# Kernel tuning notes

Measured on AMD Instinct MI355X. Metric: run time of the kernel, lower is better.

## Reference

```python
import jax, jax.numpy as jnp
import numpy as np

B, S, D_IN, UNITS = 4, 4096, 256, 64


def setup_inputs() -> dict:
    key = jax.random.key(0)
    ks = jax.random.split(key, 4)
    scale = 1.0 / np.sqrt(D_IN)
    return {
        "x": jax.random.normal(ks[0], (B, S, D_IN), dtype=jnp.float32),
        "Wq": jax.random.normal(ks[1], (D_IN, UNITS), dtype=jnp.float32) * scale,
        "bq": jnp.zeros((UNITS,), dtype=jnp.float32),
        "Wk": jax.random.normal(ks[2], (D_IN, UNITS), dtype=jnp.float32) * scale,
        "bk": jnp.zeros((UNITS,), dtype=jnp.float32),
        "Wv": jax.random.normal(ks[3], (D_IN, UNITS), dtype=jnp.float32) * scale,
        "bv": jnp.zeros((UNITS,), dtype=jnp.float32),
    }


def reference(x, Wq, bq, Wk, bk, Wv, bv):
    # Q/K/V projections: [B, S, D_IN] @ [D_IN, UNITS] -> [B, S, UNITS]
    q = jnp.einsum("bsd,du->bsu", x, Wq) + bq
    k = jnp.einsum("bsd,du->bsu", x, Wk) + bk
    v = jnp.einsum("bsd,du->bsu", x, Wv) + bv
    # Full [B, S, S] scores (the module materializes these - headroom target)
    sims = jnp.einsum("bsu,btu->bst", q, k) / np.sqrt(UNITS).astype(np.float32)
    attn = jax.nn.softmax(sims, axis=-1)
    out = jnp.einsum("bst,btu->bsu", attn, v)
    return out  # activation is None (linear)
```

## Files before the change

kernel.cpp:

```cpp
#include <hip/hip_runtime.h>
#include <hip/hip_bf16.h>

#define B_ 4
#define S_ 4096
#define D_ 256
#define U_ 64
#define NROWS (B_ * S_)
#define QSCALE 0.1803368801111244f

typedef __attribute__((ext_vector_type(8))) short short8;
typedef __attribute__((ext_vector_type(8))) float float8;
typedef __attribute__((ext_vector_type(4))) float floatx4;

__device__ inline short f2bf(float f) {
    union { __hip_bfloat16 h; short s; } u;
    u.h = __float2bfloat16(f);
    return u.s;
}
__device__ inline unsigned pk2bf(float a, float b) {
    unsigned ua = __float_as_uint(a) + 0x8000u;
    unsigned ub = __float_as_uint(b) + 0x8000u;
    return (ub & 0xFFFF0000u) | (ua >> 16);
}
__device__ inline float fast_exp2(float x) {
#if __has_builtin(__builtin_amdgcn_exp2f)
    return __builtin_amdgcn_exp2f(x);
#else
    return exp2f(x);
#endif
}

__global__ void pack_w_kernel(const float* __restrict__ Wq,
                              const float* __restrict__ Wk,
                              const float* __restrict__ Wv,
                              short* __restrict__ wpack) {
    int tid = blockIdx.x * 256 + threadIdx.x;
    if (tid >= 3 * 16384) return;
    int p = tid >> 14, e = tid & 16383;
    const float* W = (p == 0) ? Wq : (p == 1) ? Wk : Wv;
    float w = W[e];
    int k = e >> 6, n = e & 63;
    int ks = k >> 5, hi = (k >> 3) & 3, j = k & 7;
    int l = hi * 16 + (n & 15), nc = n >> 4;
    wpack[p * 16384 + ((ks * 4 + nc) * 64 + l) * 8 + j] = f2bf(w);
}

__global__ __launch_bounds__(256) void qkv_proj_kernel(
    const float* __restrict__ x, const short* __restrict__ wpack,
    const float* __restrict__ bq, const float* __restrict__ bk,
    const float* __restrict__ bv,
    short* __restrict__ Q, short* __restrict__ Kpack, short* __restrict__ Vpack) {
    __shared__ __align__(16) short k_sh[64][72];
    __shared__ __align__(16) short vT_sh[64][72];
    const int wl    = threadIdx.x >> 6;
    const int lane  = threadIdx.x & 63;
    const int col16 = lane & 15, quad = lane >> 4;
    const int m0b = blockIdx.x * 64, m0 = m0b + wl * 16;

    floatx4 acc[3][4];
#pragma unroll
    for (int p = 0; p < 3; ++p)
#pragma unroll
        for (int nc = 0; nc < 4; ++nc) acc[p][nc] = (floatx4){0.f, 0.f, 0.f, 0.f};

    const float* xrow = x + (size_t)(m0 + col16) * D_ + quad * 8;
#pragma unroll
    for (int ks = 0; ks < 8; ++ks) {
        float8 af = *(const float8*)(xrow + ks * 32);
        short8 a;
#pragma unroll
        for (int j = 0; j < 8; ++j) a[j] = f2bf(af[j]);
#pragma unroll
        for (int p = 0; p < 3; ++p) {
#pragma unroll
            for (int nc = 0; nc < 4; ++nc) {
                short8 bfr = *(const short8*)(wpack +
                    ((size_t)((p * 8 + ks) * 4 + nc) * 64 + lane) * 8);
                acc[p][nc] = __builtin_amdgcn_mfma_f32_16x16x32_bf16(a, bfr, acc[p][nc], 0, 0, 0);
            }
        }
    }

#pragma unroll
    for (int nc = 0; nc < 4; ++nc) {
        float biasq = bq[nc * 16 + col16];
        float biask = bk[nc * 16 + col16];
        float biasv = bv[nc * 16 + col16];
#pragma unroll
        for (int r = 0; r < 4; ++r) {
            int row = m0 + quad * 4 + r;
            Q[(size_t)row * U_ + nc * 16 + col16] = f2bf((acc[0][nc][r] + biasq) * QSCALE);
            k_sh[wl * 16 + quad * 4 + r][nc * 16 + col16] = f2bf(acc[1][nc][r] + biask);
        }
        union { short s[4]; unsigned long long u; } pv;
#pragma unroll
        for (int r = 0; r < 4; ++r) pv.s[r] = f2bf(acc[2][nc][r] + biasv);
        *(unsigned long long*)&vT_sh[nc * 16 + col16][wl * 16 + quad * 4] = pv.u;
    }
    __syncthreads();

#pragma unroll
    for (int c2 = 0; c2 < 2; ++c2) {
        int combo = wl + c2 * 4;
        int ww = combo >> 2, t = (combo >> 1) & 1, h = combo & 1;
        int srow = ww * 32 + (col16 >> 2) * 8 + (col16 & 3) + 4 * t;
        short8 v = *(const short8*)&k_sh[srow][h * 32 + quad * 8];
        size_t gt = (size_t)blockIdx.x * 2 + ww;
        *(short8*)(Kpack + (gt * 4 + t * 2 + h) * 512 + lane * 8) = v;
    }
#pragma unroll
    for (int c2 = 0; c2 < 2; ++c2) {
        int combo = wl + c2 * 4;
        int ww = combo >> 2, nc = combo & 3;
        short8 v = *(const short8*)&vT_sh[nc * 16 + col16][ww * 32 + quad * 8];
        size_t gt = (size_t)blockIdx.x * 2 + ww;
        *(short8*)(Vpack + (gt * 4 + nc) * 512 + lane * 8) = v;
    }
}

__global__ __launch_bounds__(512) void attn_kernel(
    const short* __restrict__ Q, const short* __restrict__ Kpack,
    const short* __restrict__ Vpack, float* __restrict__ out) {
    __shared__ float o_sh[4][32][65];
    __shared__ float l_sh[8][2][16];

    const int i  = blockIdx.x;
    const int b  = (i & 7) >> 1;
    const int q0 = ((((i >> 3) << 1) | (i & 1))) * 32;
    const int kw = threadIdx.x >> 6;
    const int lane  = threadIdx.x & 63;
    const int col16 = lane & 15, quad = lane >> 4;

    const short* Qb = Q + (size_t)b * S_ * U_;

    short8 bQ[2][2];
#pragma unroll
    for (int qs = 0; qs < 2; ++qs) {
        const short* qrow = Qb + (size_t)(q0 + qs * 16 + col16) * U_ + quad * 8;
        bQ[qs][0] = *(const short8*)(qrow);
        bQ[qs][1] = *(const short8*)(qrow + 32);
    }

    floatx4 o[2][4];
#pragma unroll
    for (int qs = 0; qs < 2; ++qs)
#pragma unroll
        for (int nc = 0; nc < 4; ++nc) o[qs][nc] = (floatx4){0.f, 0.f, 0.f, 0.f};
    float l_i[2] = {0.f, 0.f};

    const short* kbase = Kpack + ((size_t)(b * 128 + kw * 16)) * 2048 + lane * 8;
    const short* vbase = Vpack + ((size_t)(b * 128 + kw * 16)) * 2048 + lane * 8;

    for (int it = 0; it < 16; ++it) {
        const short* kp = kbase + it * 2048;
        const short* vp = vbase + it * 2048;
        short8 ak[2][2];
#pragma unroll
        for (int t = 0; t < 2; ++t)
#pragma unroll
            for (int h = 0; h < 2; ++h)
                ak[t][h] = *(const short8*)(kp + (t * 2 + h) * 512);
        short8 av[4];
#pragma unroll
        for (int nc = 0; nc < 4; ++nc)
            av[nc] = *(const short8*)(vp + nc * 512);

        floatx4 c[2][2];
#pragma unroll
        for (int t = 0; t < 2; ++t)
#pragma unroll
            for (int qs = 0; qs < 2; ++qs) {
                c[t][qs] = __builtin_amdgcn_mfma_f32_16x16x32_bf16(ak[t][0], bQ[qs][0],
                              (floatx4){0.f, 0.f, 0.f, 0.f}, 0, 0, 0);
                c[t][qs] = __builtin_amdgcn_mfma_f32_16x16x32_bf16(ak[t][1], bQ[qs][1], c[t][qs], 0, 0, 0);
            }

#pragma unroll
        for (int qs = 0; qs < 2; ++qs) {
            float p[8];
            float rs = 0.f;
#pragma unroll
            for (int t = 0; t < 2; ++t)
#pragma unroll
                for (int r = 0; r < 4; ++r) {
                    float e = fast_exp2(c[t][qs][r]);
                    p[t * 4 + r] = e;
                    rs += e;
                }
            l_i[qs] += rs;
            union { short8 s; unsigned u[4]; } pb;
            pb.u[0] = pk2bf(p[0], p[1]);
            pb.u[1] = pk2bf(p[2], p[3]);
            pb.u[2] = pk2bf(p[4], p[5]);
            pb.u[3] = pk2bf(p[6], p[7]);
#pragma unroll
            for (int nc = 0; nc < 4; ++nc)
                o[qs][nc] = __builtin_amdgcn_mfma_f32_16x16x32_bf16(av[nc], pb.s, o[qs][nc], 0, 0, 0);
        }
    }

#pragma unroll
    for (int qs = 0; qs < 2; ++qs) {
        l_i[qs] += __shfl_xor(l_i[qs], 16, 64);
        l_i[qs] += __shfl_xor(l_i[qs], 32, 64);
    }
    if (quad == 0) {
#pragma unroll
        for (int qs = 0; qs < 2; ++qs) l_sh[kw][qs][col16] = l_i[qs];
    }

    if (kw < 4) {
#pragma unroll
        for (int qs = 0; qs < 2; ++qs)
#pragma unroll
            for (int nc = 0; nc < 4; ++nc)
#pragma unroll
                for (int r = 0; r < 4; ++r)
                    o_sh[kw][qs * 16 + col16][nc * 16 + quad * 4 + r] = o[qs][nc][r];
    }
    __syncthreads();
    if (kw >= 4) {
#pragma unroll
        for (int qs = 0; qs < 2; ++qs)
#pragma unroll
            for (int nc = 0; nc < 4; ++nc)
#pragma unroll
                for (int r = 0; r < 4; ++r)
                    o_sh[kw - 4][qs * 16 + col16][nc * 16 + quad * 4 + r] += o[qs][nc][r];
    }
    __syncthreads();
    for (int i2 = threadIdx.x; i2 < 32 * 64; i2 += 512) {
        int row = i2 >> 6, col = i2 & 63;
        int qs2 = row >> 4, c = row & 15;
        float lt = 0.f;
#pragma unroll
        for (int ww = 0; ww < 8; ++ww) lt += l_sh[ww][qs2][c];
        float s = o_sh[0][row][col] + o_sh[1][row][col]
                + o_sh[2][row][col] + o_sh[3][row][col];
        out[((size_t)b * S_ + q0 + row) * U_ + col] = s / lt;
    }
}

extern "C" void kernel_launch(void* const* d_in, const int* in_sizes, int n_in,
                              void* d_out, int out_size, void* d_ws, size_t ws_size,
                              hipStream_t stream) {
    const float* x  = (const float*)d_in[0];
    const float* Wq = (const float*)d_in[1];
    const float* bq = (const float*)d_in[2];
    const float* Wk = (const float*)d_in[3];
    const float* bk = (const float*)d_in[4];
    const float* Wv = (const float*)d_in[5];
    const float* bv = (const float*)d_in[6];
    float* out = (float*)d_out;

    short* Q     = (short*)d_ws;
    short* Kpack = Q + (size_t)NROWS * U_;
    short* Vpack = Kpack + (size_t)NROWS * U_;
    short* wpack = Vpack + (size_t)NROWS * U_;

    pack_w_kernel<<<192, 256, 0, stream>>>(Wq, Wk, Wv, wpack);
    qkv_proj_kernel<<<NROWS / 64, 256, 0, stream>>>(
        x, wpack, bq, bk, bv, Q, Kpack, Vpack);
    attn_kernel<<<512, 512, 0, stream>>>(Q, Kpack, Vpack, out);
}
```

Before: 108.1 us.

## Share K/V tiles via double-buffered LDS and split keys across blocks with merge kernel

Restructures the attention kernel so that each 256-thread block handles 64 query rows against a quarter of the keys. The block's waves cooperatively load K/V tiles into double-buffered LDS, replacing the old scheme where each wave read its own K/V chunk from global memory. Partial outputs and row sums go to workspace slabs, and a new merge kernel sums the four key-split partials and normalizes. This raises K/V reuse per block and gives more blocks. The cost is a barrier per tile, an extra kernel launch, and a round trip through global memory for 4x the output size.

```diff
diff --git a/kernel.cpp b/kernel.cpp
--- a/kernel.cpp
+++ b/kernel.cpp
@@ -118,127 +118,120 @@
     }
 }
 
-__global__ __launch_bounds__(512) void attn_kernel(
+__global__ __launch_bounds__(256) void attn_kernel(
     const short* __restrict__ Q, const short* __restrict__ Kpack,
-    const short* __restrict__ Vpack, float* __restrict__ out) {
-    __shared__ float o_sh[4][32][65];
-    __shared__ float l_sh[8][2][16];
+    const short* __restrict__ Vpack, float* __restrict__ oslab,
+    float* __restrict__ lslab) {
+    __shared__ __align__(16) short lds[2][4096];
 
     const int i  = blockIdx.x;
     const int b  = (i & 7) >> 1;
-    const int q0 = ((((i >> 3) << 1) | (i & 1))) * 32;
-    const int kw = threadIdx.x >> 6;
+    const int r  = ((i >> 3) << 1) | (i & 1);
+    const int kw = r & 3, qb = r >> 2;
+    const int w  = threadIdx.x >> 6;
     const int lane  = threadIdx.x & 63;
     const int col16 = lane & 15, quad = lane >> 4;
-
-    const short* Qb = Q + (size_t)b * S_ * U_;
-
-    short8 bQ[2][2];
-#pragma unroll
-    for (int qs = 0; qs < 2; ++qs) {
-        const short* qrow = Qb + (size_t)(q0 + qs * 16 + col16) * U_ + quad * 8;
-        bQ[qs][0] = *(const short8*)(qrow);
-        bQ[qs][1] = *(const short8*)(qrow + 32);
-    }
-
-    floatx4 o[2][4];
-#pragma unroll
-    for (int qs = 0; qs < 2; ++qs)
-#pragma unroll
-        for (int nc = 0; nc < 4; ++nc) o[qs][nc] = (floatx4){0.f, 0.f, 0.f, 0.f};
-    float l_i[2] = {0.f, 0.f};
-
-    const short* kbase = Kpack + ((size_t)(b * 128 + kw * 16)) * 2048 + lane * 8;
-    const short* vbase = Vpack + ((size_t)(b * 128 + kw * 16)) * 2048 + lane * 8;
-
-    for (int it = 0; it < 16; ++it) {
-        const short* kp = kbase + it * 2048;
-        const short* vp = vbase + it * 2048;
+    const int q0 = qb * 64 + w * 16;
+
+    const short* qrow = Q + ((size_t)(b * S_ + q0 + col16)) * U_ + quad * 8;
+    short8 bQ0 = *(const short8*)(qrow);
+    short8 bQ1 = *(const short8*)(qrow + 32);
+
+    floatx4 o[4];
+#pragma unroll
+    for (int nc = 0; nc < 4; ++nc) o[nc] = (floatx4){0.f, 0.f, 0.f, 0.f};
+    float l_i = 0.f;
+
+    const int tb = b * 128 + kw * 32;
+    const short* kg = Kpack + (size_t)tb * 2048 + w * 512 + lane * 8;
+    const short* vg = Vpack + (size_t)tb * 2048 + w * 512 + lane * 8;
+
+    short8 gk = *(const short8*)(kg);
+    short8 gv = *(const short8*)(vg);
+    *(short8*)&lds[0][w * 512 + lane * 8]        = gk;
+    *(short8*)&lds[0][2048 + w * 512 + lane * 8] = gv;
+    __syncthreads();
+
+    for (int it = 0; it < 32; ++it) {
+        const int cur = it & 1;
+        if (it + 1 < 32) {
+            gk = *(const short8*)(kg + (size_t)(it + 1) * 2048);
+            gv = *(const short8*)(vg + (size_t)(it + 1) * 2048);
+        }
+        const short* base = lds[cur];
         short8 ak[2][2];
 #pragma unroll
         for (int t = 0; t < 2; ++t)
 #pragma unroll
             for (int h = 0; h < 2; ++h)
-                ak[t][h] = *(const short8*)(kp + (t * 2 + h) * 512);
+                ak[t][h] = *(const short8*)(base + (t * 2 + h) * 512 + lane * 8);
         short8 av[4];
 #pragma unroll
         for (int nc = 0; nc < 4; ++nc)
-            av[nc] = *(const short8*)(vp + nc * 512);
-
-        floatx4 c[2][2];
+            av[nc] = *(const short8*)(base + 2048 + nc * 512 + lane * 8);
+
+        floatx4 c[2];
+#pragma unroll
+        for (int t = 0; t < 2; ++t) {
+            c[t] = __builtin_amdgcn_mfma_f32_16x16x32_bf16(ak[t][0], bQ0,
+                      (floatx4){0.f, 0.f, 0.f, 0.f}, 0, 0, 0);
+            c[t] = __builtin_amdgcn_mfma_f32_16x16x32_bf16(ak[t][1], bQ1, c[t], 0, 0, 0);
+        }
+        float p[8];
+        float rs = 0.f;
 #pragma unroll
         for (int t = 0; t < 2; ++t)
 #pragma unroll
-            for (int qs = 0; qs < 2; ++qs) {
-                c[t][qs] = __builtin_amdgcn_mfma_f32_16x16x32_bf16(ak[t][0], bQ[qs][0],
-                              (floatx4){0.f, 0.f, 0.f, 0.f}, 0, 0, 0);
-                c[t][qs] = __builtin_amdgcn_mfma_f32_16x16x32_bf16(ak[t][1], bQ[qs][1], c[t][qs], 0, 0, 0);
+            for (int rr = 0; rr < 4; ++rr) {
+                float e = fast_exp2(c[t][rr]);
+                p[t * 4 + rr] = e;
+                rs += e;
             }
-
-#pragma unroll
-        for (int qs = 0; qs < 2; ++qs) {
-            float p[8];
-            float rs = 0.f;
-#pragma unroll
-            for (int t = 0; t < 2; ++t)
-#pragma unroll
-                for (int r = 0; r < 4; ++r) {
-                    float e = fast_exp2(c[t][qs][r]);
-                    p[t * 4 + r] = e;
-                    rs += e;
-                }
-            l_i[qs] += rs;
-            union { short8 s; unsigned u[4]; } pb;
-            pb.u[0] = pk2bf(p[0], p[1]);
-            pb.u[1] = pk2bf(p[2], p[3]);
-            pb.u[2] = pk2bf(p[4], p[5]);
-            pb.u[3] = pk2bf(p[6], p[7]);
-#pragma unroll
-            for (int nc = 0; nc < 4; ++nc)
-                o[qs][nc] = __builtin_amdgcn_mfma_f32_16x16x32_bf16(av[nc], pb.s, o[qs][nc], 0, 0, 0);
-        }
-    }
-
-#pragma unroll
-    for (int qs = 0; qs < 2; ++qs) {
-        l_i[qs] += __shfl_xor(l_i[qs], 16, 64);
-        l_i[qs] += __shfl_xor(l_i[qs], 32, 64);
-    }
-    if (quad == 0) {
-#pragma unroll
-        for (int qs = 0; qs < 2; ++qs) l_sh[kw][qs][col16] = l_i[qs];
-    }
-
-    if (kw < 4) {
-#pragma unroll
-        for (int qs = 0; qs < 2; ++qs)
-#pragma unroll
-            for (int nc = 0; nc < 4; ++nc)
-#pragma unroll
-                for (int r = 0; r < 4; ++r)
-                    o_sh[kw][qs * 16 + col16][nc * 16 + quad * 4 + r] = o[qs][nc][r];
-    }
-    __syncthreads();
-    if (kw >= 4) {
-#pragma unroll
-        for (int qs = 0; qs < 2; ++qs)
-#pragma unroll
-            for (int nc = 0; nc < 4; ++nc)
-#pragma unroll
-                for (int r = 0; r < 4; ++r)
-                    o_sh[kw - 4][qs * 16 + col16][nc * 16 + quad * 4 + r] += o[qs][nc][r];
-    }
-    __syncthreads();
-    for (int i2 = threadIdx.x; i2 < 32 * 64; i2 += 512) {
-        int row = i2 >> 6, col = i2 & 63;
-        int qs2 = row >> 4, c = row & 15;
-        float lt = 0.f;
-#pragma unroll
-        for (int ww = 0; ww < 8; ++ww) lt += l_sh[ww][qs2][c];
-        float s = o_sh[0][row][col] + o_sh[1][row][col]
-                + o_sh[2][row][col] + o_sh[3][row][col];
-        out[((size_t)b * S_ + q0 + row) * U_ + col] = s / lt;
-    }
+        l_i += rs;
+        union { short8 s; unsigned u[4]; } pb;
+        pb.u[0] = pk2bf(p[0], p[1]);
+        pb.u[1] = pk2bf(p[2], p[3]);
+        pb.u[2] = pk2bf(p[4], p[5]);
+        pb.u[3] = pk2bf(p[6], p[7]);
+#pragma unroll
+        for (int nc = 0; nc < 4; ++nc)
+            o[nc] = __builtin_amdgcn_mfma_f32_16x16x32_bf16(av[nc], pb.s, o[nc], 0, 0, 0);
+
+        if (it + 1 < 32) {
+            *(short8*)&lds[cur ^ 1][w * 512 + lane * 8]        = gk;
+            *(short8*)&lds[cur ^ 1][2048 + w * 512 + lane * 8] = gv;
+        }
+        __syncthreads();
+    }
+
+    l_i += __shfl_xor(l_i, 16, 64);
+    l_i += __shfl_xor(l_i, 32, 64);
+    if (quad == 0)
+        lslab[(size_t)kw * NROWS + b * S_ + q0 + col16] = l_i;
+
+    float* fl = (float*)lds + w * 1024;
+#pragma unroll
+    for (int nc = 0; nc < 4; ++nc)
+#pragma unroll
+        for (int rr = 0; rr < 4; ++rr)
+            fl[col16 * 64 + nc * 16 + quad * 4 + rr] = o[nc][rr];
+    asm volatile("s_waitcnt lgkmcnt(0)" ::: "memory");
+    float* dst = oslab + ((size_t)kw * NROWS + b * S_ + q0) * U_ + lane * 16;
+#pragma unroll
+    for (int v4 = 0; v4 < 4; ++v4)
+        *(float4*)(dst + v4 * 4) = *(float4*)(fl + lane * 16 + v4 * 4);
+}
+
+__global__ __launch_bounds__(256) void merge_kernel(
+    const float* __restrict__ oslab, const float* __restrict__ lslab,
+    float* __restrict__ out) {
+    int idx = blockIdx.x * 256 + threadIdx.x;
+    int row = idx >> 6;
+    float s = oslab[idx] + oslab[idx + (size_t)NROWS * 64]
+            + oslab[idx + (size_t)2 * NROWS * 64] + oslab[idx + (size_t)3 * NROWS * 64];
+    float l = lslab[row] + lslab[row + NROWS]
+            + lslab[row + 2 * NROWS] + lslab[row + 3 * NROWS];
+    out[idx] = s / l;
 }
 
 extern "C" void kernel_launch(void* const* d_in, const int* in_sizes, int n_in,
@@ -257,9 +250,12 @@
     short* Kpack = Q + (size_t)NROWS * U_;
     short* Vpack = Kpack + (size_t)NROWS * U_;
     short* wpack = Vpack + (size_t)NROWS * U_;
+    float* oslab = (float*)(wpack + 65536);
+    float* lslab = oslab + (size_t)4 * NROWS * 64;
 
     pack_w_kernel<<<192, 256, 0, stream>>>(Wq, Wk, Wv, wpack);
     qkv_proj_kernel<<<NROWS / 64, 256, 0, stream>>>(
         x, wpack, bq, bk, bv, Q, Kpack, Vpack);
-    attn_kernel<<<512, 512, 0, stream>>>(Q, Kpack, Vpack, out);
-}
+    attn_kernel<<<1024, 256, 0, stream>>>(Q, Kpack, Vpack, oslab, lslab);
+    merge_kernel<<<NROWS * 64 / 256, 256, 0, stream>>>(oslab, lslab, out);
+}
```

Result: slower. 121.4 us (+12.3%).
